# Kernel optimization log

Hardware: AMD Instinct MI355X
Metric: run time of the kernel (lower is better)

The kernel has to match this reference:

```python
import jax, jax.numpy as jnp
import numpy as np

H = 16
D_K = 64  # d_model // h = 1024 // 16
LN_EPS = 1e-5


def _layernorm(x, gamma, beta):
    mu = jnp.mean(x, axis=-1, keepdims=True)
    var = jnp.var(x, axis=-1, keepdims=True)
    return (x - mu) * jax.lax.rsqrt(var + LN_EPS) * gamma + beta


def setup_inputs() -> dict:
    key = jax.random.key(0)
    ks = jax.random.split(key, 4)
    B, S, D = 4, 2048, 1024
    scale = 1.0 / np.sqrt(D)
    return {
        "x": jax.random.normal(ks[0], (B, S, D), dtype=jnp.float32),
        "Wq": jax.random.normal(ks[1], (D, D), dtype=jnp.float32) * scale,
        "bq": jnp.zeros((D,), dtype=jnp.float32),
        "Wk": jax.random.normal(ks[2], (D, D), dtype=jnp.float32) * scale,
        "bk": jnp.zeros((D,), dtype=jnp.float32),
        "Wv": jax.random.normal(ks[3], (D, D), dtype=jnp.float32) * scale,
        "bv": jnp.zeros((D,), dtype=jnp.float32),
        "ln_gamma": jnp.ones((D,), dtype=jnp.float32),
        "ln_beta": jnp.zeros((D,), dtype=jnp.float32),
    }


def reference(x, Wq, bq, Wk, bk, Wv, bv, ln_gamma, ln_beta):
    B, S, D = x.shape
    xn = _layernorm(x, ln_gamma, ln_beta)
    # nn.Linear: y = x @ W.T + b
    q = (xn @ Wq.T + bq).reshape(B, S, H, D_K).transpose(0, 2, 1, 3)  # [B,H,S,d_k]
    k = (xn @ Wk.T + bk).reshape(B, S, H, D_K).transpose(0, 2, 1, 3)
    v = (xn @ Wv.T + bv).reshape(B, S, H, D_K).transpose(0, 2, 1, 3)
    scores = jnp.einsum("bhqd,bhkd->bhqk", q, k) / jnp.sqrt(jnp.float32(D_K))
    p_attn = jax.nn.softmax(scores, axis=-1)
    out = jnp.einsum("bhqk,bhkd->bhqd", p_attn, v)  # [B,H,S,d_k]
    out = out.transpose(0, 2, 1, 3).reshape(B, S, H * D_K)
    # dropout is identity in eval mode
    return out
```

## Files before the change

kernel.cpp:

```cpp
#include <hip/hip_runtime.h>
#include <cstdint>
#include <cstddef>


typedef __attribute__((ext_vector_type(8))) __bf16 bf16x8;
typedef __attribute__((ext_vector_type(4))) float f32x4;
typedef __attribute__((ext_vector_type(16))) float f32x16;
typedef __attribute__((ext_vector_type(4))) unsigned int u32x4;

#define LOG2E 1.4426950408889634f
#define QSCALE (0.125f * LOG2E)

static __device__ __forceinline__ unsigned short f2bf(float f) {
  union { float f; unsigned int u; } v; v.f = f;
  unsigned int r = v.u + 0x7fffu + ((v.u >> 16) & 1u);
  return (unsigned short)(r >> 16);
}

static __device__ __forceinline__ void gload16(const void* g, void* l) {
  __builtin_amdgcn_global_load_lds(
      (const __attribute__((address_space(1))) unsigned int*)g,
      (__attribute__((address_space(3))) unsigned int*)l, 16, 0, 0);
}

static __device__ __forceinline__ f32x4 mfma16(bf16x8 a, bf16x8 b, f32x4 c) {
  return __builtin_amdgcn_mfma_f32_16x16x32_bf16(a, b, c, 0, 0, 0);
}

static __device__ __forceinline__ f32x16 mfma32(bf16x8 a, bf16x8 b, f32x16 c) {
  return __builtin_amdgcn_mfma_f32_32x32x16_bf16(a, b, c, 0, 0, 0);
}

static __device__ __forceinline__ unsigned int cvtpk(float lo, float hi) {
  unsigned int r;
  asm("v_cvt_pk_bf16_f32 %0, %1, %2" : "=v"(r) : "v"(lo), "v"(hi));
  return r;
}

static __device__ __forceinline__ void swap32(unsigned int& a, unsigned int& b) {
  asm("v_permlane32_swap_b32 %0, %1" : "+v"(a), "+v"(b));
}

__global__ __launch_bounds__(256) void ln_kernel(
    const float* __restrict__ x, const float* __restrict__ gamma,
    const float* __restrict__ beta, unsigned short* __restrict__ xn) {
  const int row = blockIdx.x;
  const int t = threadIdx.x;
  const float4 v = ((const float4*)(x + (size_t)row * 1024))[t];
  float s = v.x + v.y + v.z + v.w;
  float sq = v.x * v.x + v.y * v.y + v.z * v.z + v.w * v.w;
#pragma unroll
  for (int o = 1; o < 64; o <<= 1) { s += __shfl_xor(s, o); sq += __shfl_xor(sq, o); }
  __shared__ float red[2][4];
  const int lane = t & 63, w = t >> 6;
  if (lane == 0) { red[0][w] = s; red[1][w] = sq; }
  __syncthreads();
  s = red[0][0] + red[0][1] + red[0][2] + red[0][3];
  sq = red[1][0] + red[1][1] + red[1][2] + red[1][3];
  const float mean = s * (1.0f / 1024.0f);
  const float var = sq * (1.0f / 1024.0f) - mean * mean;
  const float rs = rsqrtf(var + 1e-5f);
  const float4 g4 = ((const float4*)gamma)[t];
  const float4 b4 = ((const float4*)beta)[t];
  ushort4 o4;
  o4.x = f2bf((v.x - mean) * rs * g4.x + b4.x);
  o4.y = f2bf((v.y - mean) * rs * g4.y + b4.y);
  o4.z = f2bf((v.z - mean) * rs * g4.z + b4.z);
  o4.w = f2bf((v.w - mean) * rs * g4.w + b4.w);
  ((ushort4*)(xn + (size_t)row * 1024))[t] = o4;
}

__global__ __launch_bounds__(256) void wconv_kernel(
    const float* __restrict__ Wq, const float* __restrict__ Wk,
    const float* __restrict__ Wv, unsigned short* __restrict__ Wcat) {
  const int idx = blockIdx.x * 256 + threadIdx.x;
  const int which = idx >> 18;
  const int off = (idx & 262143) << 2;
  const float* src = which == 0 ? Wq : (which == 1 ? Wk : Wv);
  const float sc = which == 0 ? QSCALE : 1.0f;
  float4 v = *(const float4*)(src + off);
  ushort4 o;
  o.x = f2bf(v.x * sc); o.y = f2bf(v.y * sc);
  o.z = f2bf(v.z * sc); o.w = f2bf(v.w * sc);
  *(ushort4*)(Wcat + ((size_t)which << 20) + off) = o;
}

__global__ __launch_bounds__(256) void qkv_gemm(
    const unsigned short* __restrict__ xn, const unsigned short* __restrict__ Wcat,
    const float* __restrict__ bq, const float* __restrict__ bk,
    const float* __restrict__ bv, unsigned short* __restrict__ Q,
    unsigned short* __restrict__ K, unsigned short* __restrict__ V) {
  __shared__ __align__(16) unsigned short Ash[128 * 64];
  __shared__ __align__(16) unsigned short Bsh[128 * 64];
  const int m0 = blockIdx.x * 128;
  const int n0 = blockIdx.y * 128;
  const int t = threadIdx.x;
  const int lane = t & 63, w = t >> 6;
  const int wr = w >> 1, wc = w & 1;
  const int c15 = lane & 15, g = lane >> 4;
  f32x4 acc[4][4] = {};
  for (int kt = 0; kt < 16; ++kt) {
#pragma unroll
    for (int i = 0; i < 4; ++i) {
      const int li = i * 256 + t;
      const int row = li >> 3, ck = li & 7;
      gload16(xn + (size_t)(m0 + row) * 1024 + kt * 64 + ck * 8,
              &Ash[(i * 256 + w * 64) * 8]);
      gload16(Wcat + (size_t)(n0 + row) * 1024 + kt * 64 + ck * 8,
              &Bsh[(i * 256 + w * 64) * 8]);
    }
    __syncthreads();
#pragma unroll
    for (int ks = 0; ks < 2; ++ks) {
      bf16x8 af[4], bfv[4];
#pragma unroll
      for (int mi = 0; mi < 4; ++mi)
        af[mi] = *(const bf16x8*)&Ash[(wr * 64 + mi * 16 + c15) * 64 + ks * 32 + g * 8];
#pragma unroll
      for (int ni = 0; ni < 4; ++ni)
        bfv[ni] = *(const bf16x8*)&Bsh[(wc * 64 + ni * 16 + c15) * 64 + ks * 32 + g * 8];
#pragma unroll
      for (int mi = 0; mi < 4; ++mi)
#pragma unroll
        for (int ni = 0; ni < 4; ++ni)
          acc[mi][ni] = mfma16(af[mi], bfv[ni], acc[mi][ni]);
    }
    __syncthreads();
  }
  const int nsel = n0 >> 10;
  const float* bias = nsel == 0 ? bq : (nsel == 1 ? bk : bv);
  unsigned short* dst = nsel == 0 ? Q : (nsel == 1 ? K : V);
  const float bscale = nsel == 0 ? QSCALE : 1.0f;
#pragma unroll
  for (int ni = 0; ni < 4; ++ni) {
    const int ncol = (n0 & 1023) + wc * 64 + ni * 16 + c15;
    const float bb = bias[ncol] * bscale;
    const int h = ncol >> 6, dk = ncol & 63;
#pragma unroll
    for (int mi = 0; mi < 4; ++mi) {
#pragma unroll
      for (int r = 0; r < 4; ++r) {
        const int m = m0 + wr * 64 + mi * 16 + g * 4 + r;
        const int b = m >> 11, sI = m & 2047;
        dst[((size_t)((b * 16 + h) * 2048 + sI)) * 64 + dk] = f2bf(acc[mi][ni][r] + bb);
      }
    }
  }
}

__global__ __launch_bounds__(256) void vt_kernel(
    const unsigned short* __restrict__ V, unsigned short* __restrict__ Vt) {
  __shared__ unsigned short tile[64][65];
  const int st = blockIdx.x, bh = blockIdx.y;
  const int t = threadIdx.x;
  const unsigned short* Vb = V + ((size_t)bh * 2048 + st * 64) * 64;
#pragma unroll
  for (int i = 0; i < 2; ++i) {
    const int li = i * 256 + t;
    const int s = li >> 3, c = li & 7;
    ushort4 a = *(const ushort4*)(Vb + s * 64 + c * 8);
    ushort4 b = *(const ushort4*)(Vb + s * 64 + c * 8 + 4);
    tile[s][c * 8 + 0] = a.x; tile[s][c * 8 + 1] = a.y;
    tile[s][c * 8 + 2] = a.z; tile[s][c * 8 + 3] = a.w;
    tile[s][c * 8 + 4] = b.x; tile[s][c * 8 + 5] = b.y;
    tile[s][c * 8 + 6] = b.z; tile[s][c * 8 + 7] = b.w;
  }
  __syncthreads();
  unsigned short* dst = Vt + (size_t)bh * 64 * 2048 + st * 64;
#pragma unroll
  for (int i = 0; i < 2; ++i) {
    const int li = i * 256 + t;
    const int d = li >> 3, c = li & 7;
    ushort4 o1, o2;
    o1.x = tile[c * 8 + 0][d]; o1.y = tile[c * 8 + 1][d];
    o1.z = tile[c * 8 + 2][d]; o1.w = tile[c * 8 + 3][d];
    o2.x = tile[c * 8 + 4][d]; o2.y = tile[c * 8 + 5][d];
    o2.z = tile[c * 8 + 6][d]; o2.w = tile[c * 8 + 7][d];
    *(ushort4*)(dst + (size_t)d * 2048 + c * 8) = o1;
    *(ushort4*)(dst + (size_t)d * 2048 + c * 8 + 4) = o2;
  }
}

__global__ __launch_bounds__(512) void attn_kernel(
    const unsigned short* __restrict__ Q, const unsigned short* __restrict__ K,
    const unsigned short* __restrict__ Vt, float* __restrict__ out) {
  __shared__ __align__(16) unsigned short Ksh[3][64 * 64];
  __shared__ __align__(16) unsigned short Vsh[3][64 * 64];
  const int id = blockIdx.x;
  const int k7 = id >> 3;
  const int qt = k7 & 7, bh = (id & 7) + 8 * (k7 >> 3);
  const int t = threadIdx.x, lane = t & 63, w = t >> 6;
  const int l31 = lane & 31, hi = lane >> 5;
  const int b = bh >> 4, h = bh & 15;
  const unsigned short* Qb = Q + (size_t)bh * 2048 * 64;
  const unsigned short* Kb = K + (size_t)bh * 2048 * 64;
  const unsigned short* Vb = Vt + (size_t)bh * 64 * 2048;
  const int q0w = qt * 256 + w * 32;
  bf16x8 qf[4];
#pragma unroll
  for (int ds = 0; ds < 4; ++ds)
    qf[ds] = *(const bf16x8*)(Qb + (size_t)(q0w + l31) * 64 + ds * 16 + hi * 8);
  bf16x8 ones;
#pragma unroll
  for (int j = 0; j < 8; ++j) ones[j] = (__bf16)1.0f;
  f32x16 oacc[2] = {};
  f32x16 lacc = {};

  const int sl31 = t & 31, shi = (t >> 5) & 1;
  const int skb = t >> 8, sds = (t >> 6) & 3;
  const int sks = t >> 7, sdb = (t >> 6) & 1;
  const unsigned short* Ksrc = Kb + (size_t)(skb * 32 + sl31) * 64 + (sds * 2 + shi) * 8;
  const unsigned short* Vsrc = Vb + (size_t)(sdb * 32 + sl31) * 2048 + (sks * 2 + shi) * 8;

#define STAGE(kvt, bb)                                       \
  {                                                          \
    gload16(Ksrc + (size_t)(kvt) * 4096, &Ksh[bb][w * 512]); \
    gload16(Vsrc + (size_t)(kvt) * 64, &Vsh[bb][w * 512]);   \
  }

  STAGE(0, 0);
  STAGE(1, 1);
  int bufc = 0;
  for (int kv = 0; kv < 32; ++kv) {
    if (kv == 31) {
      asm volatile("s_waitcnt vmcnt(0)" ::: "memory");
    } else {
      asm volatile("s_waitcnt vmcnt(2)" ::: "memory");
    }
    __builtin_amdgcn_s_barrier();
    bf16x8 pa[4];
#pragma unroll
    for (int kb = 0; kb < 2; ++kb) {
      f32x16 s = {};
      __builtin_amdgcn_s_setprio(1);
#pragma unroll
      for (int ds = 0; ds < 4; ++ds) {
        bf16x8 ak = *(const bf16x8*)&Ksh[bufc][((kb * 4 + ds) * 64 + lane) * 8];
        s = mfma32(ak, qf[ds], s);
      }
      __builtin_amdgcn_s_setprio(0);
      unsigned int wd[8];
#pragma unroll
      for (int i = 0; i < 8; ++i)
        wd[i] = cvtpk(__builtin_amdgcn_exp2f(s[2 * i]),
                      __builtin_amdgcn_exp2f(s[2 * i + 1]));
      swap32(wd[0], wd[2]); swap32(wd[1], wd[3]);
      swap32(wd[4], wd[6]); swap32(wd[5], wd[7]);
      const u32x4 fa = {wd[0], wd[1], wd[2], wd[3]};
      const u32x4 fb = {wd[4], wd[5], wd[6], wd[7]};
      pa[kb * 2]     = __builtin_bit_cast(bf16x8, fa);
      pa[kb * 2 + 1] = __builtin_bit_cast(bf16x8, fb);
    }
    __builtin_amdgcn_s_setprio(1);
#pragma unroll
    for (int ks = 0; ks < 4; ++ks) {
      lacc = mfma32(pa[ks], ones, lacc);
#pragma unroll
      for (int db = 0; db < 2; ++db) {
        bf16x8 bv8 = *(const bf16x8*)&Vsh[bufc][((ks * 2 + db) * 64 + lane) * 8];
        oacc[db] = mfma32(pa[ks], bv8, oacc[db]);
      }
    }
    __builtin_amdgcn_s_setprio(0);
    if (kv + 2 < 32) {
      int nb = bufc + 2; if (nb >= 3) nb -= 3;
      STAGE(kv + 2, nb);
    }
    bufc = (bufc + 1 == 3) ? 0 : bufc + 1;
  }
#undef STAGE
#pragma unroll
  for (int r = 0; r < 16; ++r) {
    const float inv = 1.0f / lacc[r];
    const int q = q0w + (r & 3) + 8 * (r >> 2) + 4 * hi;
    const size_t base = ((size_t)(b * 2048 + q)) * 1024 + h * 64;
    out[base + l31] = oacc[0][r] * inv;
    out[base + 32 + l31] = oacc[1][r] * inv;
  }
}

extern "C" void kernel_launch(void* const* d_in, const int* in_sizes, int n_in,
                              void* d_out, int out_size, void* d_ws, size_t ws_size,
                              hipStream_t stream) {
  const float* x   = (const float*)d_in[0];
  const float* Wq  = (const float*)d_in[1];
  const float* bq  = (const float*)d_in[2];
  const float* Wk  = (const float*)d_in[3];
  const float* bk  = (const float*)d_in[4];
  const float* Wv  = (const float*)d_in[5];
  const float* bv  = (const float*)d_in[6];
  const float* gam = (const float*)d_in[7];
  const float* bet = (const float*)d_in[8];

  unsigned short* ws   = (unsigned short*)d_ws;
  unsigned short* xn   = ws;
  unsigned short* Wcat = xn + 8192 * 1024;
  unsigned short* Qb   = Wcat + 3072 * 1024;
  unsigned short* Kb   = Qb + 64 * 2048 * 64;
  unsigned short* Vb   = Kb + 64 * 2048 * 64;
  unsigned short* Vtb  = Vb + 64 * 2048 * 64;
  float* outp = (float*)d_out;

  hipLaunchKernelGGL(ln_kernel, dim3(8192), dim3(256), 0, stream, x, gam, bet, xn);
  hipLaunchKernelGGL(wconv_kernel, dim3(3072), dim3(256), 0, stream, Wq, Wk, Wv, Wcat);
  hipLaunchKernelGGL(qkv_gemm, dim3(64, 24), dim3(256), 0, stream,
                     xn, Wcat, bq, bk, bv, Qb, Kb, Vb);
  hipLaunchKernelGGL(vt_kernel, dim3(32, 64), dim3(256), 0, stream, Vb, Vtb);
  hipLaunchKernelGGL(attn_kernel, dim3(512), dim3(512), 0, stream, Qb, Kb, Vtb, outp);
}
```

Before: 172.0 us.

## Double-buffer QKV GEMM loads with fragment-ordered LDS and XCD-aware tile mapping

Result: slower. 195.7 us (+13.8%).

```diff
diff --git a/kernel.cpp b/kernel.cpp
--- a/kernel.cpp
+++ b/kernel.cpp
@@ -90,43 +90,65 @@
     const float* __restrict__ bq, const float* __restrict__ bk,
     const float* __restrict__ bv, unsigned short* __restrict__ Q,
     unsigned short* __restrict__ K, unsigned short* __restrict__ V) {
-  __shared__ __align__(16) unsigned short Ash[128 * 64];
-  __shared__ __align__(16) unsigned short Bsh[128 * 64];
-  const int m0 = blockIdx.x * 128;
-  const int n0 = blockIdx.y * 128;
+  __shared__ __align__(16) unsigned short Ash[2][128 * 64];
+  __shared__ __align__(16) unsigned short Bsh[2][128 * 64];
+  const int xcd = blockIdx.x & 7, blk = blockIdx.x >> 3;
+  const int m0 = (blk & 63) * 128;
+  const int n0 = (xcd * 3 + (blk >> 6)) * 128;
   const int t = threadIdx.x;
   const int lane = t & 63, w = t >> 6;
   const int wr = w >> 1, wc = w & 1;
   const int c15 = lane & 15, g = lane >> 4;
+  int soff[4];
+#pragma unroll
+  for (int i = 0; i < 4; ++i) {
+    const int frag = i * 4 + w;
+    soff[i] = ((frag >> 1) * 16 + c15) * 1024 + (frag & 1) * 32 + g * 8;
+  }
+  const unsigned short* Axn = xn + (size_t)m0 * 1024;
+  const unsigned short* Bwc = Wcat + (size_t)n0 * 1024;
+
+#define GSTAGE(ktv, bb)                                               \
+  {                                                                   \
+    _Pragma("unroll") for (int i = 0; i < 4; ++i) {                   \
+      gload16(Axn + soff[i] + (ktv) * 64, &Ash[bb][(i * 256 + w * 64) * 8]); \
+      gload16(Bwc + soff[i] + (ktv) * 64, &Bsh[bb][(i * 256 + w * 64) * 8]); \
+    }                                                                 \
+  }
+
   f32x4 acc[4][4] = {};
+  GSTAGE(0, 0);
+  GSTAGE(1, 1);
   for (int kt = 0; kt < 16; ++kt) {
-#pragma unroll
-    for (int i = 0; i < 4; ++i) {
-      const int li = i * 256 + t;
-      const int row = li >> 3, ck = li & 7;
-      gload16(xn + (size_t)(m0 + row) * 1024 + kt * 64 + ck * 8,
-              &Ash[(i * 256 + w * 64) * 8]);
-      gload16(Wcat + (size_t)(n0 + row) * 1024 + kt * 64 + ck * 8,
-              &Bsh[(i * 256 + w * 64) * 8]);
-    }
-    __syncthreads();
+    const int cb = kt & 1;
+    if (kt == 15) {
+      asm volatile("s_waitcnt vmcnt(0)" ::: "memory");
+    } else {
+      asm volatile("s_waitcnt vmcnt(8)" ::: "memory");
+    }
+    __builtin_amdgcn_s_barrier();
+    __builtin_amdgcn_s_setprio(1);
 #pragma unroll
     for (int ks = 0; ks < 2; ++ks) {
       bf16x8 af[4], bfv[4];
 #pragma unroll
       for (int mi = 0; mi < 4; ++mi)
-        af[mi] = *(const bf16x8*)&Ash[(wr * 64 + mi * 16 + c15) * 64 + ks * 32 + g * 8];
+        af[mi] = *(const bf16x8*)&Ash[cb][(((wr * 4 + mi) * 2 + ks) * 64 + lane) * 8];
 #pragma unroll
       for (int ni = 0; ni < 4; ++ni)
-        bfv[ni] = *(const bf16x8*)&Bsh[(wc * 64 + ni * 16 + c15) * 64 + ks * 32 + g * 8];
+        bfv[ni] = *(const bf16x8*)&Bsh[cb][(((wc * 4 + ni) * 2 + ks) * 64 + lane) * 8];
 #pragma unroll
       for (int mi = 0; mi < 4; ++mi)
 #pragma unroll
         for (int ni = 0; ni < 4; ++ni)
           acc[mi][ni] = mfma16(af[mi], bfv[ni], acc[mi][ni]);
     }
-    __syncthreads();
-  }
+    __builtin_amdgcn_s_setprio(0);
+    asm volatile("s_waitcnt lgkmcnt(0)" ::: "memory");
+    __builtin_amdgcn_s_barrier();
+    if (kt + 2 < 16) GSTAGE(kt + 2, cb);
+  }
+#undef GSTAGE
   const int nsel = n0 >> 10;
   const float* bias = nsel == 0 ? bq : (nsel == 1 ? bk : bv);
   unsigned short* dst = nsel == 0 ? Q : (nsel == 1 ? K : V);
@@ -303,7 +325,7 @@
 
   hipLaunchKernelGGL(ln_kernel, dim3(8192), dim3(256), 0, stream, x, gam, bet, xn);
   hipLaunchKernelGGL(wconv_kernel, dim3(3072), dim3(256), 0, stream, Wq, Wk, Wv, Wcat);
-  hipLaunchKernelGGL(qkv_gemm, dim3(64, 24), dim3(256), 0, stream,
+  hipLaunchKernelGGL(qkv_gemm, dim3(1536), dim3(256), 0, stream,
                      xn, Wcat, bq, bk, bv, Qb, Kb, Vb);
   hipLaunchKernelGGL(vt_kernel, dim3(32, 64), dim3(256), 0, stream, Vb, Vtb);
   hipLaunchKernelGGL(attn_kernel, dim3(512), dim3(512), 0, stream, Qb, Kb, Vtb, outp);
```

## Restructure QKV GEMM with triple-buffered LDS pipeline and 32x32 MFMA tiles

Applied to the files above, without the earlier changes.

Result: no change. 170.5 us (-0.9%).

```diff
diff --git a/kernel.cpp b/kernel.cpp
--- a/kernel.cpp
+++ b/kernel.cpp
@@ -21,10 +21,6 @@
   __builtin_amdgcn_global_load_lds(
       (const __attribute__((address_space(1))) unsigned int*)g,
       (__attribute__((address_space(3))) unsigned int*)l, 16, 0, 0);
-}
-
-static __device__ __forceinline__ f32x4 mfma16(bf16x8 a, bf16x8 b, f32x4 c) {
-  return __builtin_amdgcn_mfma_f32_16x16x32_bf16(a, b, c, 0, 0, 0);
 }
 
 static __device__ __forceinline__ f32x16 mfma32(bf16x8 a, bf16x8 b, f32x16 c) {
@@ -85,64 +81,77 @@
   *(ushort4*)(Wcat + ((size_t)which << 20) + off) = o;
 }
 
-__global__ __launch_bounds__(256) void qkv_gemm(
+__global__ __launch_bounds__(512, 4) void qkv_gemm(
     const unsigned short* __restrict__ xn, const unsigned short* __restrict__ Wcat,
     const float* __restrict__ bq, const float* __restrict__ bk,
     const float* __restrict__ bv, unsigned short* __restrict__ Q,
     unsigned short* __restrict__ K, unsigned short* __restrict__ V) {
-  __shared__ __align__(16) unsigned short Ash[128 * 64];
-  __shared__ __align__(16) unsigned short Bsh[128 * 64];
-  const int m0 = blockIdx.x * 128;
+  __shared__ __align__(16) unsigned short Ash[3][8192];
+  __shared__ __align__(16) unsigned short Bsh[3][4096];
+  const int m0 = blockIdx.x * 256;
   const int n0 = blockIdx.y * 128;
   const int t = threadIdx.x;
   const int lane = t & 63, w = t >> 6;
+  const int l31 = lane & 31, hi = lane >> 5;
   const int wr = w >> 1, wc = w & 1;
-  const int c15 = lane & 15, g = lane >> 4;
-  f32x4 acc[4][4] = {};
-  for (int kt = 0; kt < 16; ++kt) {
-#pragma unroll
-    for (int i = 0; i < 4; ++i) {
-      const int li = i * 256 + t;
-      const int row = li >> 3, ck = li & 7;
-      gload16(xn + (size_t)(m0 + row) * 1024 + kt * 64 + ck * 8,
-              &Ash[(i * 256 + w * 64) * 8]);
-      gload16(Wcat + (size_t)(n0 + row) * 1024 + kt * 64 + ck * 8,
-              &Bsh[(i * 256 + w * 64) * 8]);
-    }
-    __syncthreads();
+  const int off0 = ((w >> 1) * 32 + l31) * 1024 + (w & 1) * 16 + hi * 8;
+  const unsigned short* Asrc = xn + (size_t)m0 * 1024 + off0;
+  const unsigned short* Bsrc = Wcat + (size_t)n0 * 1024 + off0;
+
+#define GSTAGE(ktv, bb)                                          \
+  {                                                              \
+    gload16(Asrc + (ktv) * 32, &Ash[bb][w * 512]);               \
+    gload16(Asrc + 131072 + (ktv) * 32, &Ash[bb][4096 + w * 512]); \
+    gload16(Bsrc + (ktv) * 32, &Bsh[bb][w * 512]);               \
+  }
+
+  f32x16 acc[2][2] = {};
+  GSTAGE(0, 0);
+  GSTAGE(1, 1);
+  int bufc = 0;
+  for (int kt = 0; kt < 32; ++kt) {
+    if (kt == 31) {
+      asm volatile("s_waitcnt vmcnt(0)" ::: "memory");
+    } else {
+      asm volatile("s_waitcnt vmcnt(3)" ::: "memory");
+    }
+    __builtin_amdgcn_s_barrier();
+    __builtin_amdgcn_s_setprio(1);
 #pragma unroll
     for (int ks = 0; ks < 2; ++ks) {
-      bf16x8 af[4], bfv[4];
-#pragma unroll
-      for (int mi = 0; mi < 4; ++mi)
-        af[mi] = *(const bf16x8*)&Ash[(wr * 64 + mi * 16 + c15) * 64 + ks * 32 + g * 8];
-#pragma unroll
-      for (int ni = 0; ni < 4; ++ni)
-        bfv[ni] = *(const bf16x8*)&Bsh[(wc * 64 + ni * 16 + c15) * 64 + ks * 32 + g * 8];
-#pragma unroll
-      for (int mi = 0; mi < 4; ++mi)
-#pragma unroll
-        for (int ni = 0; ni < 4; ++ni)
-          acc[mi][ni] = mfma16(af[mi], bfv[ni], acc[mi][ni]);
-    }
-    __syncthreads();
-  }
+      bf16x8 a0 = *(const bf16x8*)&Ash[bufc][((wr * 4 + ks) * 64 + lane) * 8];
+      bf16x8 a1 = *(const bf16x8*)&Ash[bufc][((wr * 4 + 2 + ks) * 64 + lane) * 8];
+      bf16x8 b0 = *(const bf16x8*)&Bsh[bufc][((wc * 4 + ks) * 64 + lane) * 8];
+      bf16x8 b1 = *(const bf16x8*)&Bsh[bufc][((wc * 4 + 2 + ks) * 64 + lane) * 8];
+      acc[0][0] = mfma32(a0, b0, acc[0][0]);
+      acc[0][1] = mfma32(a0, b1, acc[0][1]);
+      acc[1][0] = mfma32(a1, b0, acc[1][0]);
+      acc[1][1] = mfma32(a1, b1, acc[1][1]);
+    }
+    __builtin_amdgcn_s_setprio(0);
+    if (kt + 2 < 32) {
+      int nb = bufc + 2; if (nb >= 3) nb -= 3;
+      GSTAGE(kt + 2, nb);
+    }
+    bufc = (bufc + 1 == 3) ? 0 : bufc + 1;
+  }
+#undef GSTAGE
   const int nsel = n0 >> 10;
   const float* bias = nsel == 0 ? bq : (nsel == 1 ? bk : bv);
   unsigned short* dst = nsel == 0 ? Q : (nsel == 1 ? K : V);
   const float bscale = nsel == 0 ? QSCALE : 1.0f;
 #pragma unroll
-  for (int ni = 0; ni < 4; ++ni) {
-    const int ncol = (n0 & 1023) + wc * 64 + ni * 16 + c15;
-    const float bb = bias[ncol] * bscale;
-    const int h = ncol >> 6, dk = ncol & 63;
-#pragma unroll
-    for (int mi = 0; mi < 4; ++mi) {
-#pragma unroll
-      for (int r = 0; r < 4; ++r) {
-        const int m = m0 + wr * 64 + mi * 16 + g * 4 + r;
+  for (int ml = 0; ml < 2; ++ml) {
+#pragma unroll
+    for (int nl = 0; nl < 2; ++nl) {
+      const int nc = (n0 & 1023) + wc * 64 + nl * 32 + l31;
+      const float bb = bias[nc] * bscale;
+      const int h = nc >> 6, dk = nc & 63;
+#pragma unroll
+      for (int r = 0; r < 16; ++r) {
+        const int m = m0 + wr * 64 + ml * 32 + (r & 3) + 8 * (r >> 2) + 4 * hi;
         const int b = m >> 11, sI = m & 2047;
-        dst[((size_t)((b * 16 + h) * 2048 + sI)) * 64 + dk] = f2bf(acc[mi][ni][r] + bb);
+        dst[((size_t)((b * 16 + h) * 2048 + sI)) * 64 + dk] = f2bf(acc[ml][nl][r] + bb);
       }
     }
   }
@@ -303,7 +312,7 @@
 
   hipLaunchKernelGGL(ln_kernel, dim3(8192), dim3(256), 0, stream, x, gam, bet, xn);
   hipLaunchKernelGGL(wconv_kernel, dim3(3072), dim3(256), 0, stream, Wq, Wk, Wv, Wcat);
-  hipLaunchKernelGGL(qkv_gemm, dim3(64, 24), dim3(256), 0, stream,
+  hipLaunchKernelGGL(qkv_gemm, dim3(32, 24), dim3(512), 0, stream,
                      xn, Wcat, bq, bk, bv, Qb, Kb, Vb);
   hipLaunchKernelGGL(vt_kernel, dim3(32, 64), dim3(256), 0, stream, Vb, Vtb);
   hipLaunchKernelGGL(attn_kernel, dim3(512), dim3(512), 0, stream, Qb, Kb, Vtb, outp);
```
